# Performance work log

Hardware: AMD Instinct MI355X
Metric: run time of the kernel (lower is better)

Reference implementation:

```python
import jax, jax.numpy as jnp
import numpy as np
import math

HEADS = 12
D_MODEL = 768
HEAD_DIM = D_MODEL // HEADS
B, S = 2, 2048


def setup_inputs() -> dict:
    key = jax.random.key(0)
    ks = jax.random.split(key, 12)
    scale = 1.0 / math.sqrt(D_MODEL)
    inp = {
        'q': jax.random.normal(ks[0], (B, S, D_MODEL), dtype=jnp.float32),
        'k': jax.random.normal(ks[1], (B, S, D_MODEL), dtype=jnp.float32),
        'v': jax.random.normal(ks[2], (B, S, D_MODEL), dtype=jnp.float32),
        # binary padding mask: 1 = masked-out key position
        'mask': jax.random.randint(ks[3], (B, 1, 1, S), 0, 2).astype(jnp.float32),
        'Wq': jax.random.normal(ks[4], (D_MODEL, D_MODEL), dtype=jnp.float32) * scale,
        'bq': jnp.zeros((D_MODEL,), dtype=jnp.float32),
        'Wk': jax.random.normal(ks[5], (D_MODEL, D_MODEL), dtype=jnp.float32) * scale,
        'bk': jnp.zeros((D_MODEL,), dtype=jnp.float32),
        'Wv': jax.random.normal(ks[6], (D_MODEL, D_MODEL), dtype=jnp.float32) * scale,
        'bv': jnp.zeros((D_MODEL,), dtype=jnp.float32),
        'Wo': jax.random.normal(ks[7], (D_MODEL, D_MODEL), dtype=jnp.float32) * scale,
        'bo': jnp.zeros((D_MODEL,), dtype=jnp.float32),
    }
    return inp


def _split_heads(x):
    b, s, _ = x.shape
    return x.reshape(b, s, HEADS, HEAD_DIM).transpose(0, 2, 1, 3)  # [b,h,s,dh]


def reference(q, k, v, mask, Wq, bq, Wk, bk, Wv, bv, Wo, bo):
    # Linear projections (torch Linear: x @ W.T + b)
    qw = _split_heads(q @ Wq.T + bq)
    kw = _split_heads(k @ Wk.T + bk)
    vw = _split_heads(v @ Wv.T + bv)
    scores = jnp.einsum('bhqd,bhkd->bhqk', qw, kw) / math.sqrt(HEAD_DIM)
    # torch code does scores += mask * (-inf): masked (mask!=0) positions -> -inf
    scores = jnp.where(mask != 0, -jnp.inf, scores)
    weights = jax.nn.softmax(scores, axis=-1)  # [b,h,sq,sk]
    ctx = jnp.einsum('bhqk,bhkd->bhqd', weights, vw)
    ctx = ctx.transpose(0, 2, 1, 3).reshape(q.shape[0], q.shape[1], D_MODEL)
    out = ctx @ Wo.T + bo
    return out, weights
```

## Files before the change

kernel.cpp:

```cpp
#include <hip/hip_runtime.h>

typedef __bf16 bf16x8 __attribute__((ext_vector_type(8)));
typedef __bf16 bf16x4 __attribute__((ext_vector_type(4)));
typedef float  f32x4  __attribute__((ext_vector_type(4)));

#define MFMA_BF16(a, b, c) __builtin_amdgcn_mfma_f32_16x16x32_bf16((a), (b), (c), 0, 0, 0)

static constexpr int BATCH  = 2;
static constexpr int HEADS  = 12;
static constexpr int SEQ    = 2048;
static constexpr int DHEAD  = 64;
static constexpr int DMODEL = 768;
static constexpr int M_ROWS = BATCH * SEQ;
static constexpr int OUT_ELEMS  = M_ROWS * DMODEL;
static constexpr int HEAD_ELEMS = BATCH * HEADS * SEQ * DHEAD;

__device__ __forceinline__ void split_bf16(float x, __bf16 &hi, __bf16 &lo) {
    __bf16 h = (__bf16)x;
    hi = h;
    lo = (__bf16)(x - (float)h);
}

__global__ __launch_bounds__(256) void mask_scan_kernel(
    const float* __restrict__ mask, int* __restrict__ cidx, int* __restrict__ nb)
{
    const int b = blockIdx.x;
    const int tid = threadIdx.x;
    __shared__ int ssum[256];

    int loc[8];
    int run = 0;
    const int s0 = tid * 8;
    #pragma unroll
    for (int i = 0; i < 8; i++) {
        int u = (mask[b * SEQ + s0 + i] == 0.0f) ? 1 : 0;
        loc[i] = run;
        run += u;
    }
    ssum[tid] = run;
    __syncthreads();
    for (int off = 1; off < 256; off <<= 1) {
        int v = (tid >= off) ? ssum[tid - off] : 0;
        __syncthreads();
        ssum[tid] += v;
        __syncthreads();
    }
    int base = (tid == 0) ? 0 : ssum[tid - 1];
    #pragma unroll
    for (int i = 0; i < 8; i++)
        cidx[b * SEQ + s0 + i] = base + loc[i];
    if (tid == 255) nb[b] = ssum[255];
}

__global__ __launch_bounds__(256) void qkv_proj_kernel(
    const float* __restrict__ qin, const float* __restrict__ kin, const float* __restrict__ vin,
    const float* __restrict__ Wq, const float* __restrict__ bq,
    const float* __restrict__ Wk, const float* __restrict__ bk,
    const float* __restrict__ Wv, const float* __restrict__ bv,
    const float* __restrict__ mask, const int* __restrict__ cidx,
    __bf16* __restrict__ Qh_hi, __bf16* __restrict__ Qh_lo,
    __bf16* __restrict__ Kc_hi, __bf16* __restrict__ Kc_lo,
    __bf16* __restrict__ Vc_hi)
{
    const int z = blockIdx.z;
    const float* X; const float* W; const float* bias;
    float scale = 1.0f;
    if (z == 0)      { X = qin; W = Wq; bias = bq; scale = 0.125f; }
    else if (z == 1) { X = kin; W = Wk; bias = bk; }
    else             { X = vin; W = Wv; bias = bv; }

    __shared__ __bf16 As_hi[128 * 40];
    __shared__ __bf16 As_lo[128 * 40];
    __shared__ __bf16 Bs_hi[128 * 40];
    __shared__ __bf16 Bs_lo[128 * 40];

    const int tid  = threadIdx.x;
    const int wid  = tid >> 6;
    const int lane = tid & 63;
    const int quad = lane >> 4;
    const int l15  = lane & 15;
    const int wm = (wid >> 1) * 64;
    const int wn = (wid & 1) * 64;
    const int mbase = blockIdx.x * 128;
    const int nbase = blockIdx.y * 128;

    const f32x4 zf = {0.f, 0.f, 0.f, 0.f};
    f32x4 acc[4][4];
    #pragma unroll
    for (int i = 0; i < 4; i++)
        #pragma unroll
        for (int j = 0; j < 4; j++) acc[i][j] = zf;

    for (int k0 = 0; k0 < DMODEL; k0 += 32) {
        #pragma unroll
        for (int i = 0; i < 4; i++) {
            int idx = i * 256 + tid;
            int r = idx >> 3;
            int c = (idx & 7) * 4;
            float4 a4 = *(const float4*)&X[(size_t)(mbase + r) * DMODEL + k0 + c];
            float4 b4 = *(const float4*)&W[(size_t)(nbase + r) * DMODEL + k0 + c];
            float af[4] = {a4.x, a4.y, a4.z, a4.w};
            float bf[4] = {b4.x, b4.y, b4.z, b4.w};
            bf16x4 ah4, al4, bh4, bl4;
            #pragma unroll
            for (int j = 0; j < 4; j++) {
                __bf16 hi, lo;
                split_bf16(af[j], hi, lo); ah4[j] = hi; al4[j] = lo;
                split_bf16(bf[j], hi, lo); bh4[j] = hi; bl4[j] = lo;
            }
            *(bf16x4*)&As_hi[r * 40 + c] = ah4;
            *(bf16x4*)&As_lo[r * 40 + c] = al4;
            *(bf16x4*)&Bs_hi[r * 40 + c] = bh4;
            *(bf16x4*)&Bs_lo[r * 40 + c] = bl4;
        }
        __syncthreads();

        bf16x8 ah[4], al[4], bh[4], bl[4];
        #pragma unroll
        for (int f = 0; f < 4; f++) {
            int ra = (wm + f * 16 + l15) * 40 + quad * 8;
            ah[f] = *(const bf16x8*)&As_hi[ra];
            al[f] = *(const bf16x8*)&As_lo[ra];
            int rb = (wn + f * 16 + l15) * 40 + quad * 8;
            bh[f] = *(const bf16x8*)&Bs_hi[rb];
            bl[f] = *(const bf16x8*)&Bs_lo[rb];
        }
        #pragma unroll
        for (int fi = 0; fi < 4; fi++)
            #pragma unroll
            for (int fj = 0; fj < 4; fj++) {
                acc[fi][fj] = MFMA_BF16(ah[fi], bh[fj], acc[fi][fj]);
                acc[fi][fj] = MFMA_BF16(ah[fi], bl[fj], acc[fi][fj]);
                acc[fi][fj] = MFMA_BF16(al[fi], bh[fj], acc[fi][fj]);
            }
        __syncthreads();
    }

    float bvals[4];
    #pragma unroll
    for (int fj = 0; fj < 4; fj++)
        bvals[fj] = bias[nbase + wn + fj * 16 + l15];

    #pragma unroll
    for (int fi = 0; fi < 4; fi++)
        #pragma unroll
        for (int fj = 0; fj < 4; fj++)
            #pragma unroll
            for (int r = 0; r < 4; r++) {
                int m = mbase + wm + fi * 16 + quad * 4 + r;
                int n = nbase + wn + fj * 16 + l15;
                float val = (acc[fi][fj][r] + bvals[fj]) * scale;
                __bf16 hi, lo;
                split_bf16(val, hi, lo);
                int bb = m >> 11;
                int s  = m & (SEQ - 1);
                int hh = n >> 6;
                int d  = n & 63;
                int bh_ = bb * HEADS + hh;
                if (z == 0) {
                    size_t idx = ((size_t)bh_ * SEQ + s) * DHEAD + d;
                    Qh_hi[idx] = hi; Qh_lo[idx] = lo;
                } else if (z == 1) {
                    if (mask[bb * SEQ + s] == 0.0f) {
                        int sc = cidx[bb * SEQ + s];
                        size_t idx = ((size_t)bh_ * SEQ + sc) * DHEAD + d;
                        Kc_hi[idx] = hi; Kc_lo[idx] = lo;
                    }
                } else {
                    if (mask[bb * SEQ + s] == 0.0f) {
                        int sc = cidx[bb * SEQ + s];
                        size_t idx = ((size_t)bh_ * DHEAD + d) * SEQ + sc;
                        Vc_hi[idx] = hi;
                    }
                }
            }
}

__global__ __launch_bounds__(256) void attn_kernel(
    const __bf16* __restrict__ Qh_hi, const __bf16* __restrict__ Qh_lo,
    const __bf16* __restrict__ Kc_hi, const __bf16* __restrict__ Kc_lo,
    const __bf16* __restrict__ Vc_hi,
    const int* __restrict__ nb,
    float* __restrict__ wout,
    float* __restrict__ ctx,
    float* __restrict__ lsum)
{
    const int qt = blockIdx.x;
    const int h  = blockIdx.y;
    const int b  = blockIdx.z;
    const int bh = b * HEADS + h;

    const int tid  = threadIdx.x;
    const int wid  = tid >> 6;
    const int lane = tid & 63;
    const int quad = lane >> 4;
    const int l15  = lane & 15;
    const int qrow0 = qt * 64 + wid * 16;

    __shared__ __bf16 Ks_hi[64 * 72];
    __shared__ __bf16 Ks_lo[64 * 72];
    __shared__ __bf16 Vs[64 * 72];
    __shared__ __bf16 Ps[64 * 72];

    const int nbv = nb[b];
    const int ktiles = (nbv + 63) >> 6;

    bf16x8 aqh[2], aql[2];
    #pragma unroll
    for (int ks = 0; ks < 2; ks++) {
        size_t off = ((size_t)bh * SEQ + qrow0 + l15) * DHEAD + ks * 32 + quad * 8;
        aqh[ks] = *(const bf16x8*)&Qh_hi[off];
        aql[ks] = *(const bf16x8*)&Qh_lo[off];
    }

    const f32x4 zf = {0.f, 0.f, 0.f, 0.f};
    f32x4 cacc[4];
    #pragma unroll
    for (int fj = 0; fj < 4; fj++) cacc[fj] = zf;
    float lrun[4] = {};

    for (int kt = 0; kt < ktiles; kt++) {
        const int k0 = kt * 64;

        #pragma unroll
        for (int i = 0; i < 2; i++) {
            int idx = i * 256 + tid;
            int r = idx >> 3;
            int c = (idx & 7) * 8;
            size_t gk = ((size_t)bh * SEQ + k0 + r) * DHEAD + c;
            size_t gv = ((size_t)bh * DHEAD + r) * SEQ + k0 + c;
            *(bf16x8*)&Ks_hi[r * 72 + c] = *(const bf16x8*)&Kc_hi[gk];
            *(bf16x8*)&Ks_lo[r * 72 + c] = *(const bf16x8*)&Kc_lo[gk];
            *(bf16x8*)&Vs[r * 72 + c]    = *(const bf16x8*)&Vc_hi[gv];
        }
        __syncthreads();

        f32x4 sacc[4];
        #pragma unroll
        for (int fj = 0; fj < 4; fj++) sacc[fj] = zf;

        #pragma unroll
        for (int ks = 0; ks < 2; ks++) {
            bf16x8 kh[4], kl[4];
            #pragma unroll
            for (int fj = 0; fj < 4; fj++) {
                int off = (fj * 16 + l15) * 72 + ks * 32 + quad * 8;
                kh[fj] = *(const bf16x8*)&Ks_hi[off];
                kl[fj] = *(const bf16x8*)&Ks_lo[off];
            }
            #pragma unroll
            for (int fj = 0; fj < 4; fj++) {
                sacc[fj] = MFMA_BF16(aqh[ks], kh[fj], sacc[fj]);
                sacc[fj] = MFMA_BF16(aqh[ks], kl[fj], sacc[fj]);
                sacc[fj] = MFMA_BF16(aql[ks], kh[fj], sacc[fj]);
            }
        }

        float tsum[4] = {};
        #pragma unroll
        for (int fj = 0; fj < 4; fj++) {
            float bias = (k0 + fj * 16 + l15 < nbv) ? 0.0f : -1e30f;
            #pragma unroll
            for (int r = 0; r < 4; r++) {
                float s = sacc[fj][r] + bias;
                s = fminf(s, 80.0f);
                float p = __expf(s);
                int rl_ = quad * 4 + r;
                wout[((size_t)bh * SEQ + qrow0 + rl_) * SEQ + k0 + fj * 16 + l15] = p;
                Ps[(wid * 16 + rl_) * 72 + fj * 16 + l15] = (__bf16)p;
                tsum[r] += p;
            }
        }
        #pragma unroll
        for (int r = 0; r < 4; r++) {
            float t = tsum[r];
            t += __shfl_xor(t, 1);
            t += __shfl_xor(t, 2);
            t += __shfl_xor(t, 4);
            t += __shfl_xor(t, 8);
            lrun[r] += t;
        }

        #pragma unroll
        for (int ks = 0; ks < 2; ks++) {
            bf16x8 ph = *(const bf16x8*)&Ps[(wid * 16 + l15) * 72 + ks * 32 + quad * 8];
            #pragma unroll
            for (int fj = 0; fj < 4; fj++) {
                bf16x8 vh = *(const bf16x8*)&Vs[(fj * 16 + l15) * 72 + ks * 32 + quad * 8];
                cacc[fj] = MFMA_BF16(ph, vh, cacc[fj]);
            }
        }
        __syncthreads();
    }

    #pragma unroll
    for (int r = 0; r < 4; r++) {
        int rl_ = quad * 4 + r;
        int row = qrow0 + rl_;
        float lv = lrun[r];
        if (l15 == 0)
            lsum[(size_t)bh * SEQ + row] = lv;
        float inv = 1.0f / lv;
        #pragma unroll
        for (int fj = 0; fj < 4; fj++)
            ctx[((size_t)b * SEQ + row) * DMODEL + h * DHEAD + fj * 16 + l15] =
                cacc[fj][r] * inv;
    }
}

__global__ __launch_bounds__(256) void rescale_scatter_kernel(
    float* __restrict__ wout, const float* __restrict__ lsum,
    const int* __restrict__ cidx, const float* __restrict__ mask,
    const int* __restrict__ nb)
{
    const int row = blockIdx.x;
    const int b   = (row >> 11) / HEADS;
    const int tid = threadIdx.x;
    const float inv = 1.0f / lsum[row];
    const int nbv = nb[b];

    __shared__ float pl[SEQ];
    float* wrow = wout + (size_t)row * SEQ;
    #pragma unroll
    for (int i = 0; i < 8; i++) {
        int c = tid + i * 256;
        if (c < nbv) pl[c] = wrow[c];
    }
    __syncthreads();

    const float* mrow = mask + b * SEQ;
    const int*   crow = cidx + b * SEQ;
    #pragma unroll
    for (int i = 0; i < 8; i++) {
        int s = i * 256 + tid;
        float w = (mrow[s] != 0.0f) ? 0.0f : pl[crow[s]] * inv;
        wrow[s] = w;
    }
}

__global__ __launch_bounds__(256) void out_proj_kernel(
    const float* __restrict__ X, const float* __restrict__ W, const float* __restrict__ bias,
    float* __restrict__ out)
{
    __shared__ __bf16 As_hi[128 * 40];
    __shared__ __bf16 As_lo[128 * 40];
    __shared__ __bf16 Bs_hi[128 * 40];
    __shared__ __bf16 Bs_lo[128 * 40];

    const int tid  = threadIdx.x;
    const int wid  = tid >> 6;
    const int lane = tid & 63;
    const int quad = lane >> 4;
    const int l15  = lane & 15;
    const int wm = (wid >> 1) * 64;
    const int wn = (wid & 1) * 64;
    const int mbase = blockIdx.x * 128;
    const int nbase = blockIdx.y * 128;

    const f32x4 zf = {0.f, 0.f, 0.f, 0.f};
    f32x4 acc[4][4];
    #pragma unroll
    for (int i = 0; i < 4; i++)
        #pragma unroll
        for (int j = 0; j < 4; j++) acc[i][j] = zf;

    for (int k0 = 0; k0 < DMODEL; k0 += 32) {
        #pragma unroll
        for (int i = 0; i < 4; i++) {
            int idx = i * 256 + tid;
            int r = idx >> 3;
            int c = (idx & 7) * 4;
            float4 a4 = *(const float4*)&X[(size_t)(mbase + r) * DMODEL + k0 + c];
            float4 b4 = *(const float4*)&W[(size_t)(nbase + r) * DMODEL + k0 + c];
            float af[4] = {a4.x, a4.y, a4.z, a4.w};
            float bf[4] = {b4.x, b4.y, b4.z, b4.w};
            bf16x4 ah4, al4, bh4, bl4;
            #pragma unroll
            for (int j = 0; j < 4; j++) {
                __bf16 hi, lo;
                split_bf16(af[j], hi, lo); ah4[j] = hi; al4[j] = lo;
                split_bf16(bf[j], hi, lo); bh4[j] = hi; bl4[j] = lo;
            }
            *(bf16x4*)&As_hi[r * 40 + c] = ah4;
            *(bf16x4*)&As_lo[r * 40 + c] = al4;
            *(bf16x4*)&Bs_hi[r * 40 + c] = bh4;
            *(bf16x4*)&Bs_lo[r * 40 + c] = bl4;
        }
        __syncthreads();

        bf16x8 ah[4], al[4], bh[4], bl[4];
        #pragma unroll
        for (int f = 0; f < 4; f++) {
            int ra = (wm + f * 16 + l15) * 40 + quad * 8;
            ah[f] = *(const bf16x8*)&As_hi[ra];
            al[f] = *(const bf16x8*)&As_lo[ra];
            int rb = (wn + f * 16 + l15) * 40 + quad * 8;
            bh[f] = *(const bf16x8*)&Bs_hi[rb];
            bl[f] = *(const bf16x8*)&Bs_lo[rb];
        }
        #pragma unroll
        for (int fi = 0; fi < 4; fi++)
            #pragma unroll
            for (int fj = 0; fj < 4; fj++) {
                acc[fi][fj] = MFMA_BF16(ah[fi], bh[fj], acc[fi][fj]);
                acc[fi][fj] = MFMA_BF16(ah[fi], bl[fj], acc[fi][fj]);
                acc[fi][fj] = MFMA_BF16(al[fi], bh[fj], acc[fi][fj]);
            }
        __syncthreads();
    }

    float bvals[4];
    #pragma unroll
    for (int fj = 0; fj < 4; fj++)
        bvals[fj] = bias[nbase + wn + fj * 16 + l15];

    #pragma unroll
    for (int fi = 0; fi < 4; fi++)
        #pragma unroll
        for (int fj = 0; fj < 4; fj++)
            #pragma unroll
            for (int r = 0; r < 4; r++) {
                int m = mbase + wm + fi * 16 + quad * 4 + r;
                int n = nbase + wn + fj * 16 + l15;
                out[(size_t)m * DMODEL + n] = acc[fi][fj][r] + bvals[fj];
            }
}

extern "C" void kernel_launch(void* const* d_in, const int* in_sizes, int n_in,
                              void* d_out, int out_size, void* d_ws, size_t ws_size,
                              hipStream_t stream) {
    (void)in_sizes; (void)n_in; (void)out_size; (void)ws_size;

    const float* q    = (const float*)d_in[0];
    const float* k    = (const float*)d_in[1];
    const float* v    = (const float*)d_in[2];
    const float* mask = (const float*)d_in[3];
    const float* Wq   = (const float*)d_in[4];
    const float* bq   = (const float*)d_in[5];
    const float* Wk   = (const float*)d_in[6];
    const float* bk   = (const float*)d_in[7];
    const float* Wv   = (const float*)d_in[8];
    const float* bv   = (const float*)d_in[9];
    const float* Wo   = (const float*)d_in[10];
    const float* bo   = (const float*)d_in[11];

    float* out  = (float*)d_out;
    float* wout = out + (size_t)OUT_ELEMS;

    __bf16* wsb = (__bf16*)d_ws;
    __bf16* Qh_hi = wsb;
    __bf16* Qh_lo = wsb + 1 * (size_t)HEAD_ELEMS;
    __bf16* Kc_hi = wsb + 2 * (size_t)HEAD_ELEMS;
    __bf16* Kc_lo = wsb + 3 * (size_t)HEAD_ELEMS;
    __bf16* Vc_hi = wsb + 4 * (size_t)HEAD_ELEMS;
    float*  ctx   = (float*)(wsb + 5 * (size_t)HEAD_ELEMS);
    float*  lsum  = ctx + (size_t)OUT_ELEMS;
    int*    cidx  = (int*)(lsum + (size_t)BATCH * HEADS * SEQ);
    int*    nb    = cidx + (size_t)BATCH * SEQ;

    mask_scan_kernel<<<dim3(BATCH), 256, 0, stream>>>(mask, cidx, nb);

    qkv_proj_kernel<<<dim3(32, 6, 3), 256, 0, stream>>>(
        q, k, v, Wq, bq, Wk, bk, Wv, bv, mask, cidx,
        Qh_hi, Qh_lo, Kc_hi, Kc_lo, Vc_hi);

    attn_kernel<<<dim3(32, 12, 2), 256, 0, stream>>>(
        Qh_hi, Qh_lo, Kc_hi, Kc_lo, Vc_hi, nb, wout, ctx, lsum);

    rescale_scatter_kernel<<<dim3(BATCH * HEADS * SEQ), 256, 0, stream>>>(
        wout, lsum, cidx, mask, nb);

    out_proj_kernel<<<dim3(32, 6, 1), 256, 0, stream>>>(ctx, Wo, bo, out);
}
```

Baseline: 850.7 us.

## Replace key compaction and rescale pass with two-pass recompute attention

Drops the mask prefix-scan and the compacted K/V layout. The padding mask becomes a shared-memory bias over all keys. Attention now runs in two passes: the first computes context and row sums without storing weights, and the second recomputes QK^T and writes the normalized weights directly. This removes the separate rescale/scatter kernel and its full read-modify-write of the large weights tensor. In exchange, QK^T is computed twice and masked keys are no longer skipped, so matrix work roughly doubles or more.

```diff
diff --git a/kernel.cpp b/kernel.cpp
--- a/kernel.cpp
+++ b/kernel.cpp
@@ -21,46 +21,14 @@
     lo = (__bf16)(x - (float)h);
 }
 
-__global__ __launch_bounds__(256) void mask_scan_kernel(
-    const float* __restrict__ mask, int* __restrict__ cidx, int* __restrict__ nb)
-{
-    const int b = blockIdx.x;
-    const int tid = threadIdx.x;
-    __shared__ int ssum[256];
-
-    int loc[8];
-    int run = 0;
-    const int s0 = tid * 8;
-    #pragma unroll
-    for (int i = 0; i < 8; i++) {
-        int u = (mask[b * SEQ + s0 + i] == 0.0f) ? 1 : 0;
-        loc[i] = run;
-        run += u;
-    }
-    ssum[tid] = run;
-    __syncthreads();
-    for (int off = 1; off < 256; off <<= 1) {
-        int v = (tid >= off) ? ssum[tid - off] : 0;
-        __syncthreads();
-        ssum[tid] += v;
-        __syncthreads();
-    }
-    int base = (tid == 0) ? 0 : ssum[tid - 1];
-    #pragma unroll
-    for (int i = 0; i < 8; i++)
-        cidx[b * SEQ + s0 + i] = base + loc[i];
-    if (tid == 255) nb[b] = ssum[255];
-}
-
 __global__ __launch_bounds__(256) void qkv_proj_kernel(
     const float* __restrict__ qin, const float* __restrict__ kin, const float* __restrict__ vin,
     const float* __restrict__ Wq, const float* __restrict__ bq,
     const float* __restrict__ Wk, const float* __restrict__ bk,
     const float* __restrict__ Wv, const float* __restrict__ bv,
-    const float* __restrict__ mask, const int* __restrict__ cidx,
     __bf16* __restrict__ Qh_hi, __bf16* __restrict__ Qh_lo,
-    __bf16* __restrict__ Kc_hi, __bf16* __restrict__ Kc_lo,
-    __bf16* __restrict__ Vc_hi)
+    __bf16* __restrict__ Kh_hi, __bf16* __restrict__ Kh_lo,
+    __bf16* __restrict__ Vh)
 {
     const int z = blockIdx.z;
     const float* X; const float* W; const float* bias;
@@ -161,27 +129,20 @@
                     size_t idx = ((size_t)bh_ * SEQ + s) * DHEAD + d;
                     Qh_hi[idx] = hi; Qh_lo[idx] = lo;
                 } else if (z == 1) {
-                    if (mask[bb * SEQ + s] == 0.0f) {
-                        int sc = cidx[bb * SEQ + s];
-                        size_t idx = ((size_t)bh_ * SEQ + sc) * DHEAD + d;
-                        Kc_hi[idx] = hi; Kc_lo[idx] = lo;
-                    }
+                    size_t idx = ((size_t)bh_ * SEQ + s) * DHEAD + d;
+                    Kh_hi[idx] = hi; Kh_lo[idx] = lo;
                 } else {
-                    if (mask[bb * SEQ + s] == 0.0f) {
-                        int sc = cidx[bb * SEQ + s];
-                        size_t idx = ((size_t)bh_ * DHEAD + d) * SEQ + sc;
-                        Vc_hi[idx] = hi;
-                    }
+                    size_t idx = ((size_t)bh_ * DHEAD + d) * SEQ + s;
+                    Vh[idx] = hi;
                 }
             }
 }
 
-__global__ __launch_bounds__(256) void attn_kernel(
+__global__ __launch_bounds__(256) void attn_ctx_kernel(
     const __bf16* __restrict__ Qh_hi, const __bf16* __restrict__ Qh_lo,
-    const __bf16* __restrict__ Kc_hi, const __bf16* __restrict__ Kc_lo,
-    const __bf16* __restrict__ Vc_hi,
-    const int* __restrict__ nb,
-    float* __restrict__ wout,
+    const __bf16* __restrict__ Kh_hi, const __bf16* __restrict__ Kh_lo,
+    const __bf16* __restrict__ Vh,
+    const float* __restrict__ mask,
     float* __restrict__ ctx,
     float* __restrict__ lsum)
 {
@@ -201,9 +162,10 @@
     __shared__ __bf16 Ks_lo[64 * 72];
     __shared__ __bf16 Vs[64 * 72];
     __shared__ __bf16 Ps[64 * 72];
-
-    const int nbv = nb[b];
-    const int ktiles = (nbv + 63) >> 6;
+    __shared__ float bias_s[SEQ];
+
+    for (int i = tid; i < SEQ; i += 256)
+        bias_s[i] = (mask[b * SEQ + i] != 0.0f) ? -1e30f : 0.0f;
 
     bf16x8 aqh[2], aql[2];
     #pragma unroll
@@ -219,7 +181,7 @@
     for (int fj = 0; fj < 4; fj++) cacc[fj] = zf;
     float lrun[4] = {};
 
-    for (int kt = 0; kt < ktiles; kt++) {
+    for (int kt = 0; kt < SEQ / 64; kt++) {
         const int k0 = kt * 64;
 
         #pragma unroll
@@ -229,9 +191,9 @@
             int c = (idx & 7) * 8;
             size_t gk = ((size_t)bh * SEQ + k0 + r) * DHEAD + c;
             size_t gv = ((size_t)bh * DHEAD + r) * SEQ + k0 + c;
-            *(bf16x8*)&Ks_hi[r * 72 + c] = *(const bf16x8*)&Kc_hi[gk];
-            *(bf16x8*)&Ks_lo[r * 72 + c] = *(const bf16x8*)&Kc_lo[gk];
-            *(bf16x8*)&Vs[r * 72 + c]    = *(const bf16x8*)&Vc_hi[gv];
+            *(bf16x8*)&Ks_hi[r * 72 + c] = *(const bf16x8*)&Kh_hi[gk];
+            *(bf16x8*)&Ks_lo[r * 72 + c] = *(const bf16x8*)&Kh_lo[gk];
+            *(bf16x8*)&Vs[r * 72 + c]    = *(const bf16x8*)&Vh[gv];
         }
         __syncthreads();
 
@@ -259,14 +221,13 @@
         float tsum[4] = {};
         #pragma unroll
         for (int fj = 0; fj < 4; fj++) {
-            float bias = (k0 + fj * 16 + l15 < nbv) ? 0.0f : -1e30f;
+            float bias = bias_s[k0 + fj * 16 + l15];
             #pragma unroll
             for (int r = 0; r < 4; r++) {
                 float s = sacc[fj][r] + bias;
                 s = fminf(s, 80.0f);
                 float p = __expf(s);
                 int rl_ = quad * 4 + r;
-                wout[((size_t)bh * SEQ + qrow0 + rl_) * SEQ + k0 + fj * 16 + l15] = p;
                 Ps[(wid * 16 + rl_) * 72 + fj * 16 + l15] = (__bf16)p;
                 tsum[r] += p;
             }
@@ -308,33 +269,95 @@
     }
 }
 
-__global__ __launch_bounds__(256) void rescale_scatter_kernel(
-    float* __restrict__ wout, const float* __restrict__ lsum,
-    const int* __restrict__ cidx, const float* __restrict__ mask,
-    const int* __restrict__ nb)
+__global__ __launch_bounds__(256) void attn_weights_kernel(
+    const __bf16* __restrict__ Qh_hi, const __bf16* __restrict__ Qh_lo,
+    const __bf16* __restrict__ Kh_hi, const __bf16* __restrict__ Kh_lo,
+    const float* __restrict__ mask,
+    const float* __restrict__ lsum,
+    float* __restrict__ wout)
 {
-    const int row = blockIdx.x;
-    const int b   = (row >> 11) / HEADS;
-    const int tid = threadIdx.x;
-    const float inv = 1.0f / lsum[row];
-    const int nbv = nb[b];
-
-    __shared__ float pl[SEQ];
-    float* wrow = wout + (size_t)row * SEQ;
-    #pragma unroll
-    for (int i = 0; i < 8; i++) {
-        int c = tid + i * 256;
-        if (c < nbv) pl[c] = wrow[c];
-    }
-    __syncthreads();
-
-    const float* mrow = mask + b * SEQ;
-    const int*   crow = cidx + b * SEQ;
-    #pragma unroll
-    for (int i = 0; i < 8; i++) {
-        int s = i * 256 + tid;
-        float w = (mrow[s] != 0.0f) ? 0.0f : pl[crow[s]] * inv;
-        wrow[s] = w;
+    const int qt = blockIdx.x;
+    const int h  = blockIdx.y;
+    const int b  = blockIdx.z;
+    const int bh = b * HEADS + h;
+
+    const int tid  = threadIdx.x;
+    const int wid  = tid >> 6;
+    const int lane = tid & 63;
+    const int quad = lane >> 4;
+    const int l15  = lane & 15;
+    const int qrow0 = qt * 64 + wid * 16;
+
+    __shared__ __bf16 Ks_hi[64 * 72];
+    __shared__ __bf16 Ks_lo[64 * 72];
+    __shared__ float bias_s[SEQ];
+
+    for (int i = tid; i < SEQ; i += 256)
+        bias_s[i] = (mask[b * SEQ + i] != 0.0f) ? -1e30f : 0.0f;
+
+    bf16x8 aqh[2], aql[2];
+    #pragma unroll
+    for (int ks = 0; ks < 2; ks++) {
+        size_t off = ((size_t)bh * SEQ + qrow0 + l15) * DHEAD + ks * 32 + quad * 8;
+        aqh[ks] = *(const bf16x8*)&Qh_hi[off];
+        aql[ks] = *(const bf16x8*)&Qh_lo[off];
+    }
+
+    float inv[4];
+    #pragma unroll
+    for (int r = 0; r < 4; r++)
+        inv[r] = 1.0f / lsum[(size_t)bh * SEQ + qrow0 + quad * 4 + r];
+
+    const f32x4 zf = {0.f, 0.f, 0.f, 0.f};
+
+    for (int kt = 0; kt < SEQ / 64; kt++) {
+        const int k0 = kt * 64;
+
+        #pragma unroll
+        for (int i = 0; i < 2; i++) {
+            int idx = i * 256 + tid;
+            int r = idx >> 3;
+            int c = (idx & 7) * 8;
+            size_t gk = ((size_t)bh * SEQ + k0 + r) * DHEAD + c;
+            *(bf16x8*)&Ks_hi[r * 72 + c] = *(const bf16x8*)&Kh_hi[gk];
+            *(bf16x8*)&Ks_lo[r * 72 + c] = *(const bf16x8*)&Kh_lo[gk];
+        }
+        __syncthreads();
+
+        f32x4 sacc[4];
+        #pragma unroll
+        for (int fj = 0; fj < 4; fj++) sacc[fj] = zf;
+
+        #pragma unroll
+        for (int ks = 0; ks < 2; ks++) {
+            bf16x8 kh[4], kl[4];
+            #pragma unroll
+            for (int fj = 0; fj < 4; fj++) {
+                int off = (fj * 16 + l15) * 72 + ks * 32 + quad * 8;
+                kh[fj] = *(const bf16x8*)&Ks_hi[off];
+                kl[fj] = *(const bf16x8*)&Ks_lo[off];
+            }
+            #pragma unroll
+            for (int fj = 0; fj < 4; fj++) {
+                sacc[fj] = MFMA_BF16(aqh[ks], kh[fj], sacc[fj]);
+                sacc[fj] = MFMA_BF16(aqh[ks], kl[fj], sacc[fj]);
+                sacc[fj] = MFMA_BF16(aql[ks], kh[fj], sacc[fj]);
+            }
+        }
+
+        #pragma unroll
+        for (int fj = 0; fj < 4; fj++) {
+            float bias = bias_s[k0 + fj * 16 + l15];
+            #pragma unroll
+            for (int r = 0; r < 4; r++) {
+                float s = sacc[fj][r] + bias;
+                s = fminf(s, 80.0f);
+                float p = __expf(s);
+                int row = qrow0 + quad * 4 + r;
+                wout[((size_t)bh * SEQ + row) * SEQ + k0 + fj * 16 + l15] = p * inv[r];
+            }
+        }
+        __syncthreads();
     }
 }
 
@@ -450,25 +473,21 @@
     __bf16* wsb = (__bf16*)d_ws;
     __bf16* Qh_hi = wsb;
     __bf16* Qh_lo = wsb + 1 * (size_t)HEAD_ELEMS;
-    __bf16* Kc_hi = wsb + 2 * (size_t)HEAD_ELEMS;
-    __bf16* Kc_lo = wsb + 3 * (size_t)HEAD_ELEMS;
-    __bf16* Vc_hi = wsb + 4 * (size_t)HEAD_ELEMS;
+    __bf16* Kh_hi = wsb + 2 * (size_t)HEAD_ELEMS;
+    __bf16* Kh_lo = wsb + 3 * (size_t)HEAD_ELEMS;
+    __bf16* Vh    = wsb + 4 * (size_t)HEAD_ELEMS;
     float*  ctx   = (float*)(wsb + 5 * (size_t)HEAD_ELEMS);
     float*  lsum  = ctx + (size_t)OUT_ELEMS;
-    int*    cidx  = (int*)(lsum + (size_t)BATCH * HEADS * SEQ);
-    int*    nb    = cidx + (size_t)BATCH * SEQ;
-
-    mask_scan_kernel<<<dim3(BATCH), 256, 0, stream>>>(mask, cidx, nb);
 
     qkv_proj_kernel<<<dim3(32, 6, 3), 256, 0, stream>>>(
-        q, k, v, Wq, bq, Wk, bk, Wv, bv, mask, cidx,
-        Qh_hi, Qh_lo, Kc_hi, Kc_lo, Vc_hi);
-
-    attn_kernel<<<dim3(32, 12, 2), 256, 0, stream>>>(
-        Qh_hi, Qh_lo, Kc_hi, Kc_lo, Vc_hi, nb, wout, ctx, lsum);
-
-    rescale_scatter_kernel<<<dim3(BATCH * HEADS * SEQ), 256, 0, stream>>>(
-        wout, lsum, cidx, mask, nb);
+        q, k, v, Wq, bq, Wk, bk, Wv, bv,
+        Qh_hi, Qh_lo, Kh_hi, Kh_lo, Vh);
+
+    attn_ctx_kernel<<<dim3(32, 12, 2), 256, 0, stream>>>(
+        Qh_hi, Qh_lo, Kh_hi, Kh_lo, Vh, mask, ctx, lsum);
+
+    attn_weights_kernel<<<dim3(32, 12, 2), 256, 0, stream>>>(
+        Qh_hi, Qh_lo, Kh_hi, Kh_lo, mask, lsum, wout);
 
     out_proj_kernel<<<dim3(32, 6, 1), 256, 0, stream>>>(ctx, Wo, bo, out);
 }
```

Result: faster. 726.3 us (-14.6%).
